# Kernel tuning notes

Measured on AMD Instinct MI355X. Metric: run time of the kernel, lower is better.

## Reference

```python
import jax, jax.numpy as jnp
import numpy as np

N_EMB = 8192
EMB_DIM = 128
BETA = 0.25


def setup_inputs() -> dict:
    key = jax.random.key(0)
    k1, k2 = jax.random.split(key)
    x = jax.random.normal(k1, (32, EMB_DIM, 1024), dtype=jnp.float32)
    embeddings = jax.random.normal(k2, (N_EMB, EMB_DIM), dtype=jnp.float32)
    return {"x": x, "embeddings": embeddings}


def reference(x, embeddings):
    # preprocess: swap chn_dim(=1) with last dim, flatten to tokens
    xt = jnp.swapaxes(x, 1, -1)                      # [B, L, D]
    flat = xt.reshape(-1, EMB_DIM)                   # [N, D]
    prenorm = jnp.linalg.norm(flat - jnp.mean(flat)) / np.sqrt(float(flat.size))

    # squared-euclidean distances via matmul + norms: [N, n_emb]
    s1 = jnp.sum(flat * flat, axis=1, keepdims=True)
    s2 = jnp.sum(embeddings * embeddings, axis=1)
    sim = flat @ embeddings.T
    distances = s1 + s2 - 2.0 * sim

    min_distance = jnp.min(distances, axis=1)
    idx = jnp.argmin(distances, axis=1)              # [N] int
    fit = jnp.mean(jnp.nan_to_num(min_distance))

    # EMA scatter statistics (one-hot matmul in torch == segment_sum here)
    k_sum = jax.ops.segment_sum(flat, idx, num_segments=N_EMB)         # [n_emb, D]
    k_elem = jax.ops.segment_sum(jnp.ones_like(idx, jnp.float32), idx,
                                 num_segments=N_EMB)                   # [n_emb]
    k_prob = k_elem / jnp.sum(k_elem)
    entropy = -jnp.sum(k_prob * jnp.log(k_prob + 1e-8))

    # embedding gather, reshape back to channels-first
    quantized = embeddings[idx].reshape(xt.shape)    # [B, L, D]
    quantized = jnp.swapaxes(quantized, 1, -1)       # [B, D, L]

    # ema_update=True -> codebook_loss = 0, only commit loss
    commit_loss = BETA * jnp.mean((jax.lax.stop_gradient(quantized) - x) ** 2)
    loss = commit_loss

    # straight-through estimator
    out = x + jax.lax.stop_gradient(quantized - x)
    return out, quantized, loss, fit, prenorm, entropy, k_sum, k_elem
```

## Files before the change

### kernel.cpp

```cpp
#include <hip/hip_runtime.h>
#include <math.h>
#include <float.h>

#define BB 32
#define DD 128
#define LL 1024
#define NN 32768
#define NE 8192
#define XSZ 4194304
#define OUT_OFF_Q     4194304
#define OUT_OFF_SCAL  8388608
#define OUT_OFF_KSUM  8388612
#define OUT_OFF_KELEM 9437188

typedef unsigned int u32;
typedef unsigned short u16;
typedef int   i32x4 __attribute__((ext_vector_type(4)));
typedef float f32x4 __attribute__((ext_vector_type(4)));

__device__ inline float waveSum(float v){
  #pragma unroll
  for (int o = 32; o > 0; o >>= 1) v += __shfl_down(v, o, 64);
  return v;
}
__device__ inline double waveSumD(double v){
  #pragma unroll
  for (int o = 32; o > 0; o >>= 1) v += __shfl_down(v, o, 64);
  return v;
}

__global__ __launch_bounds__(256) void prep_kernel(const float* __restrict__ e,
    u16* __restrict__ eh8, int* __restrict__ s2seed, float* __restrict__ s2f,
    int* __restrict__ cnt, float* __restrict__ accs)
{
  int t = threadIdx.x;
  if (blockIdx.x < 32) cnt[blockIdx.x * 256 + t] = 0;
  if (blockIdx.x == 32 && t < 16) accs[t] = 0.f;

  int row = blockIdx.x * 4 + (t >> 6);
  int kd  = t & 63;
  float2 ev = *reinterpret_cast<const float2*>(&e[row * DD + kd * 2]);
  int e0 = __float2int_rn(ev.x * 4096.f);
  int e1 = __float2int_rn(ev.y * 4096.f);
  e0 = min(max(e0, -32639), 32639);
  e1 = min(max(e1, -32639), 32639);
  double sq = (double)e0 * (double)e0 + (double)e1 * (double)e1;
  sq = waveSumD(sq);
  float sqf = ev.x * ev.x + ev.y * ev.y;
  sqf = waveSum(sqf);
  if (kd == 0){
    int sd = (int)(sq * (1.0 / 131072.0));
    sd = min(sd, 120000);
    s2seed[row] = -sd;
    s2f[row] = sqf;
  }
  int h0 = (e0 + 128) >> 8;
  int h1 = (e1 + 128) >> 8;
  int k = kd * 2;
  int T16 = row >> 4, lr = row & 15;
  int kt2 = k >> 6, lg = (k >> 4) & 3, j = k & 15;
  int du16 = (((T16*2 + kt2) * 1024) + lg*256 + lr*16 + j) >> 1;
  eh8[du16] = (u16)((h0 & 255) | ((h1 & 255) << 8));
}

#define LOADSET(AH0,AH1,SEED,TT) \
  { int T_ = (TT); \
    AH0 = *(const i32x4*)(ehp + (size_t)(T_*2 + 0) * 256); \
    AH1 = *(const i32x4*)(ehp + (size_t)(T_*2 + 1) * 256); \
    SEED = s2s4[T_*4 + sofs]; }

#define MFMA2S(SLOT, CT, AH0,AH1,SEED) \
  SLOT = __builtin_amdgcn_mfma_i32_16x16x64_i8(AH0, Bh[CT][0], SEED, 0,0,0); \
  SLOT = __builtin_amdgcn_mfma_i32_16x16x64_i8(AH1, Bh[CT][1], SLOT, 0,0,0);

#define KEYS1(T1V, CT, JV) \
  { _Pragma("unroll") \
    for (int r = 0; r < 4; ++r){ \
      int key = (int)(((u32)T1V[r] << 13) + (u32)(JV[r])); \
      int k2n; \
      asm("v_med3_i32 %0, %1, %2, %3" \
          : "=v"(k2n) : "v"(key), "v"(k1[CT]), "v"(k2[CT])); \
      k2[CT] = k2n; \
      k1[CT] = max(key, k1[CT]); \
    } }

#define TILE_BODY(AH0,AH1,SEED,JV) \
  MFMA2S(sa, 0, AH0,AH1,SEED) \
  MFMA2S(sb, 1, AH0,AH1,SEED) \
  KEYS1(sa, 0, JV) \
  MFMA2S(sa, 2, AH0,AH1,SEED) \
  KEYS1(sb, 1, JV) \
  MFMA2S(sb, 3, AH0,AH1,SEED) \
  KEYS1(sa, 2, JV) \
  KEYS1(sb, 3, JV)

__global__ __launch_bounds__(256, 4) void argmin_mfma(
    const float* __restrict__ x,
    const u32* __restrict__ eh8,
    const i32x4* __restrict__ s2s4,
    int* __restrict__ idx1o, int* __restrict__ idx2o)
{
  __shared__ int kk1[1024];
  __shared__ int kk2[1024];

  int t  = threadIdx.x;
  int w  = t >> 6;
  int l  = t & 63;
  int lr = l & 15;
  int lg = l >> 4;

  int blk  = blockIdx.x;
  int half = blk >> 9;
  int tb   = blk & 511;
  int hb64 = half * 64;

  int n0 = tb * 64;
  int b  = n0 >> 10;
  int l0 = n0 & 1023;
  const float* xb = x + (size_t)b * (DD * LL);

  i32x4 Bh[4][2];
  #pragma unroll
  for (int ct = 0; ct < 4; ++ct){
    int tok = l0 + ct*16 + lr;
    #pragma unroll
    for (int kt = 0; kt < 2; ++kt){
      #pragma unroll
      for (int dw = 0; dw < 4; ++dw){
        u32 hw = 0;
        #pragma unroll
        for (int bb = 0; bb < 4; ++bb){
          int k = kt*64 + lg*16 + dw*4 + bb;
          int xi = __float2int_rn(xb[(size_t)k * LL + tok] * 4096.f);
          xi = min(max(xi, -32639), 32639);
          int h  = (xi + 128) >> 8;
          hw |= ((u32)h & 255u) << (8*bb);
        }
        Bh[ct][kt][dw] = (int)hw;
      }
    }
  }

  int k1[4], k2[4];
  #pragma unroll
  for (int ct = 0; ct < 4; ++ct){ k1[ct] = (int)0x80000000; k2[ct] = (int)0x80000000; }

  int jvA[4], jvB[4];
  #pragma unroll
  for (int r = 0; r < 4; ++r){
    jvA[r] = 8191 - (hb64*64 + w*16 + lg*4 + r);
    jvB[r] = jvA[r] - 64;
  }

  const u32* ehp = eh8 + (size_t)l * 4;
  int sofs = lg;

  i32x4 Ah0A, Ah1A, seedA;
  i32x4 Ah0B, Ah1B, seedB;
  i32x4 sa, sb;

  LOADSET(Ah0A, Ah1A, seedA, (hb64 + 0)*4 + w)
  LOADSET(Ah0B, Ah1B, seedB, (hb64 + 1)*4 + w)

  for (int it = 0; it < 64; it += 2){
    TILE_BODY(Ah0A, Ah1A, seedA, jvA)
    if (it + 2 < 64){
      LOADSET(Ah0A, Ah1A, seedA, (hb64 + it + 2)*4 + w)
    }
    #pragma unroll
    for (int r = 0; r < 4; ++r) jvA[r] -= 128;

    TILE_BODY(Ah0B, Ah1B, seedB, jvB)
    if (it + 3 < 64){
      LOADSET(Ah0B, Ah1B, seedB, (hb64 + it + 3)*4 + w)
    }
    #pragma unroll
    for (int r = 0; r < 4; ++r) jvB[r] -= 128;
  }

  #pragma unroll
  for (int ct = 0; ct < 4; ++ct){
    int sidx = (ct*16 + lr)*16 + w*4 + lg;
    kk1[sidx] = k1[ct];
    kk2[sidx] = k2[ct];
  }
  __syncthreads();
  if (t < 64){
    int K1 = (int)0x80000000, K2 = (int)0x80000000;
    #pragma unroll 4
    for (int s = 0; s < 16; ++s){
      int a = kk1[t*16 + s], b2 = kk2[t*16 + s];
      int mn = min(a, K1);  K2 = max(mn, K2);  K1 = max(a, K1);
      mn = min(b2, K1);     K2 = max(mn, K2);  K1 = max(b2, K1);
    }
    idx1o[half*NN + n0 + t] = 8191 - (K1 & 8191);
    idx2o[half*NN + n0 + t] = 8191 - (K2 & 8191);
  }
}

__global__ __launch_bounds__(256) void fixup_kernel(const float* __restrict__ x,
    const float* __restrict__ e, const float* __restrict__ s2f,
    const int* __restrict__ idx1, const int* __restrict__ idx2,
    int* __restrict__ idxf, int* __restrict__ cnt, float* __restrict__ accs,
    float* __restrict__ out, float* __restrict__ quant, float* __restrict__ xT)
{
  __shared__ float red[5][4][64];
  __shared__ int jws[64];

  int t = threadIdx.x;
  int w = t >> 6, l = t & 63;
  int n0 = blockIdx.x * 64;
  int n  = n0 + l;
  int b  = n0 >> 10;
  int l0 = n0 & 1023;
  size_t base = (size_t)b * (DD * LL) + l0 + l;
  const float* xb = x + base;

  int js[4];
  js[0] = idx1[n];      js[1] = idx2[n];
  js[2] = idx1[NN + n]; js[3] = idx2[NN + n];

  float s1 = 0.f, sx = 0.f;
  float dt0 = 0.f, dt1 = 0.f, dt2 = 0.f, dt3 = 0.f;
  int kbase = w * 32;
  #pragma unroll
  for (int k4 = 0; k4 < 8; ++k4){
    int k = kbase + k4*4;
    float x0 = xb[(size_t)(k+0) * LL];
    float x1 = xb[(size_t)(k+1) * LL];
    float x2 = xb[(size_t)(k+2) * LL];
    float x3 = xb[(size_t)(k+3) * LL];
    s1 = fmaf(x0,x0, fmaf(x1,x1, fmaf(x2,x2, fmaf(x3,x3, s1))));
    sx += x0 + x1 + x2 + x3;
    if (xT) *(float4*)&xT[(size_t)n * DD + k] = make_float4(x0,x1,x2,x3);
    float4 v0 = *(const float4*)&e[(size_t)js[0] * DD + k];
    float4 v1 = *(const float4*)&e[(size_t)js[1] * DD + k];
    float4 v2 = *(const float4*)&e[(size_t)js[2] * DD + k];
    float4 v3 = *(const float4*)&e[(size_t)js[3] * DD + k];
    dt0 = fmaf(x0,v0.x, fmaf(x1,v0.y, fmaf(x2,v0.z, fmaf(x3,v0.w, dt0))));
    dt1 = fmaf(x0,v1.x, fmaf(x1,v1.y, fmaf(x2,v1.z, fmaf(x3,v1.w, dt1))));
    dt2 = fmaf(x0,v2.x, fmaf(x1,v2.y, fmaf(x2,v2.z, fmaf(x3,v2.w, dt2))));
    dt3 = fmaf(x0,v3.x, fmaf(x1,v3.y, fmaf(x2,v3.z, fmaf(x3,v3.w, dt3))));
  }
  red[0][w][l] = s1;
  red[1][w][l] = dt0;  red[2][w][l] = dt1;
  red[3][w][l] = dt2;  red[4][w][l] = dt3;
  sx = waveSum(sx);
  if (l == 0) atomicAdd(&accs[0], sx);
  __syncthreads();

  if (w == 0){
    float S1 = red[0][0][l] + red[0][1][l] + red[0][2][l] + red[0][3][l];
    float D[4];
    #pragma unroll
    for (int i = 0; i < 4; ++i)
      D[i] = red[1+i][0][l] + red[1+i][1][l] + red[1+i][2][l] + red[1+i][3][l];
    int jw = js[0];
    float dw = S1 + s2f[js[0]] - 2.f * D[0];
    #pragma unroll
    for (int i = 1; i < 4; ++i){
      float di = S1 + s2f[js[i]] - 2.f * D[i];
      if (di < dw || (di == dw && js[i] < jw)) { dw = di; jw = js[i]; }
    }
    idxf[n] = jw;
    atomicAdd(&cnt[jw], 1);
    jws[l] = jw;
    float S1s = waveSum(S1);
    float dws = waveSum(dw);
    if (l == 0){
      atomicAdd(&accs[1], S1s);
      atomicAdd(&accs[3], dws);
    }
  }
  __syncthreads();

  int jw = jws[l];
  float* ob = out   + base;
  float* qb = quant + base;
  #pragma unroll
  for (int k4 = 0; k4 < 8; ++k4){
    int k = kbase + k4*4;
    float4 q = *(const float4*)&e[(size_t)jw * DD + k];
    ob[(size_t)(k+0)*LL] = q.x;  qb[(size_t)(k+0)*LL] = q.x;
    ob[(size_t)(k+1)*LL] = q.y;  qb[(size_t)(k+1)*LL] = q.y;
    ob[(size_t)(k+2)*LL] = q.z;  qb[(size_t)(k+2)*LL] = q.z;
    ob[(size_t)(k+3)*LL] = q.w;  qb[(size_t)(k+3)*LL] = q.w;
  }
}

__global__ __launch_bounds__(1024) void prefix_kernel(const int* __restrict__ cnt,
    int* __restrict__ cursor, float* __restrict__ kelem,
    const float* __restrict__ accs, float* __restrict__ scal)
{
  __shared__ int sc[1024];
  __shared__ double er[16];
  int t = threadIdx.x;
  int c[8]; int s = 0;
  #pragma unroll
  for (int i = 0; i < 8; ++i){ c[i] = cnt[t*8 + i]; s += c[i]; }
  sc[t] = s;
  __syncthreads();
  for (int off = 1; off < 1024; off <<= 1){
    int v = sc[t];
    int u = (t >= off) ? sc[t - off] : 0;
    __syncthreads();
    sc[t] = v + u;
    __syncthreads();
  }
  int base = t ? sc[t-1] : 0;
  #pragma unroll
  for (int i = 0; i < 8; ++i){
    cursor[t*8 + i] = base;
    kelem[t*8 + i] = (float)c[i];
    base += c[i];
  }
  double es = 0.0;
  #pragma unroll
  for (int i = 0; i < 8; ++i){
    float p = (float)c[i] * (1.0f / NN);
    es += (double)(p * logf(p + 1e-8f));
  }
  es = waveSumD(es);
  if ((t & 63) == 0) er[t >> 6] = es;
  __syncthreads();
  if (t == 0){
    double ent = 0.0;
    #pragma unroll
    for (int i = 0; i < 16; ++i) ent += er[i];
    ent = -ent;
    float sum = accs[0], sq = accs[1], fitsum = accs[3];
    double mu  = (double)sum / (double)XSZ;
    double var = (double)sq / (double)XSZ - mu * mu;
    if (var < 0) var = 0;
    scal[0] = (float)(0.25 * (double)fitsum / (double)XSZ);
    scal[1] = (float)((double)fitsum / (double)NN);
    scal[2] = (float)sqrt(var);
    scal[3] = (float)ent;
  }
}

__global__ __launch_bounds__(256) void scatter_kernel(const int* __restrict__ idxf,
    int* __restrict__ cursor, int* __restrict__ order, int* __restrict__ jsorted,
    float* __restrict__ ksum)
{
  int n = blockIdx.x * 256 + threadIdx.x;
  {
    const float4 z = make_float4(0.f,0.f,0.f,0.f);
    float4* kz = (float4*)&ksum[(size_t)n * 32];
    #pragma unroll
    for (int i = 0; i < 8; ++i) kz[i] = z;
  }
  int j = idxf[n];
  int p = atomicAdd(&cursor[j], 1);
  order[p] = n;
  jsorted[p] = j;
}

__global__ __launch_bounds__(256) void ksum_chunk_kernel(const float* __restrict__ xT,
    const int* __restrict__ order, const int* __restrict__ jsorted,
    float* __restrict__ ksum)
{
  int wv = threadIdx.x >> 6, lane = threadIdx.x & 63;
  int chunk = blockIdx.x * 4 + wv;
  int st = chunk * 16;
  int myo = order[st + (lane & 15)];
  int myj = jsorted[st + (lane & 15)];
  float a0 = 0.f, a1 = 0.f;
  bool inside = false;
  #pragma unroll
  for (int k = 0; k < 16; ++k){
    int j = __shfl(myj, k);
    int n = __shfl(myo, k);
    const float* xr = xT + (size_t)n * DD;
    a0 += xr[lane];
    a1 += xr[64 + lane];
    int jn = (k < 15) ? __shfl(myj, k + 1) : -1;
    if (jn != j){
      if (inside && k < 15){
        ksum[j * DD + lane]      = a0;
        ksum[j * DD + 64 + lane] = a1;
      } else {
        atomicAdd(&ksum[j * DD + lane], a0);
        atomicAdd(&ksum[j * DD + 64 + lane], a1);
      }
      a0 = 0.f; a1 = 0.f;
      inside = true;
    }
  }
}

__global__ __launch_bounds__(256) void ksum_kernel(const float* __restrict__ x,
    const int* __restrict__ order, const int* __restrict__ cnt,
    const int* __restrict__ cursor, float* __restrict__ ksum)
{
  int w = threadIdx.x >> 6, lane = threadIdx.x & 63;
  int j = blockIdx.x * 4 + w;
  int c = cnt[j];
  int st = cursor[j] - c;
  float a0 = 0.f, a1 = 0.f;
  for (int k = 0; k < c; ++k){
    int n = order[st + k];
    int b = n >> 10, l = n & 1023;
    const float* xb = x + (size_t)b * (DD * LL) + l;
    a0 += xb[lane * LL];
    a1 += xb[(lane + 64) * LL];
  }
  ksum[j * DD + lane]      = a0;
  ksum[j * DD + 64 + lane] = a1;
}

extern "C" void kernel_launch(void* const* d_in, const int* in_sizes, int n_in,
                              void* d_out, int out_size, void* d_ws, size_t ws_size,
                              hipStream_t stream)
{
  const float* x = (const float*)d_in[0];
  const float* e = (const float*)d_in[1];
  float* out   = (float*)d_out;
  float* quant = out + OUT_OFF_Q;
  float* scal  = out + OUT_OFF_SCAL;
  float* ksum  = out + OUT_OFF_KSUM;
  float* kelem = out + OUT_OFF_KELEM;

  char* wsb = (char*)d_ws;
  u16*   eh8     = (u16*)(wsb);
  float* s2f     = (float*)(wsb + 1048576);
  int*   s2seed  = (int*)(wsb + 2097152);
  int*   idx1    = (int*)(wsb + 2129920);
  int*   idx2    = (int*)(wsb + 2392064);
  int*   idxf    = (int*)(wsb + 2654208);
  int*   cnt     = (int*)(wsb + 2785280);
  int*   cursor  = (int*)(wsb + 2818048);
  int*   order   = (int*)(wsb + 2850816);
  int*   jsorted = (int*)(wsb + 2981888);
  float* accs    = (float*)(wsb + 3112960);
  float* xT      = (float*)(wsb + 4194304);
  bool useXT = ws_size >= (size_t)(4194304 + 16777216);

  prep_kernel   <<<NE / 4,     256, 0, stream>>>(e, eh8, s2seed, s2f, cnt, accs);
  argmin_mfma   <<<1024,       256, 0, stream>>>(x, (const u32*)eh8,
                                                 (const i32x4*)s2seed, idx1, idx2);
  fixup_kernel  <<<NN / 64,    256, 0, stream>>>(x, e, s2f, idx1, idx2, idxf, cnt,
                                                 accs, out, quant,
                                                 useXT ? xT : (float*)nullptr);
  prefix_kernel <<<1,         1024, 0, stream>>>(cnt, cursor, kelem, accs, scal);
  scatter_kernel<<<NN / 256,   256, 0, stream>>>(idxf, cursor, order, jsorted, ksum);
  if (useXT){
    ksum_chunk_kernel<<<NN / 64, 256, 0, stream>>>(xT, order, jsorted, ksum);
  } else {
    ksum_kernel      <<<NE / 4,  256, 0, stream>>>(x, order, cnt, cursor, ksum);
  }
}
```

Measured before the change: 152.1 us.

## Pre-reduce argmin keys per row group, move xT transpose to LDS kernel, widen ksum chunks

The argmin inner loop now takes the max over four rows' packed keys with v_max3 before a single med3/max top-2 update per column tile, instead of four separate updates. Row offsets are folded into the scores as small subtractions, which keeps one index base per lane. The xT transpose moves out of fixup, where each thread did strided float4 stores, into a separate LDS-tiled kernel that also zeroes ksum. ksum chunks grow from 16 to 32 tokens per wave. Pre-reducing four rows before the top-2 update can drop a genuine second-best candidate when both best and runner-up come from the same four-row group, which may change the fixup result. The extra launch also adds overhead.

```diff
diff --git a/kernel.cpp b/kernel.cpp
--- a/kernel.cpp
+++ b/kernel.cpp
@@ -73,26 +73,29 @@
   SLOT = __builtin_amdgcn_mfma_i32_16x16x64_i8(AH0, Bh[CT][0], SEED, 0,0,0); \
   SLOT = __builtin_amdgcn_mfma_i32_16x16x64_i8(AH1, Bh[CT][1], SLOT, 0,0,0);
 
-#define KEYS1(T1V, CT, JV) \
-  { _Pragma("unroll") \
-    for (int r = 0; r < 4; ++r){ \
-      int key = (int)(((u32)T1V[r] << 13) + (u32)(JV[r])); \
-      int k2n; \
-      asm("v_med3_i32 %0, %1, %2, %3" \
-          : "=v"(k2n) : "v"(key), "v"(k1[CT]), "v"(k2[CT])); \
-      k2[CT] = k2n; \
-      k1[CT] = max(key, k1[CT]); \
-    } }
-
-#define TILE_BODY(AH0,AH1,SEED,JV) \
+#define KEYS1(T1V, CT, J) \
+  { int q0 = (int)((u32)T1V[0] << 13); \
+    int q1 = (int)((u32)T1V[1] << 13) - 1; \
+    int q2 = (int)((u32)T1V[2] << 13) - 2; \
+    int q3 = (int)((u32)T1V[3] << 13) - 3; \
+    int m; \
+    asm("v_max3_i32 %0, %1, %2, %3" : "=v"(m) : "v"(q0), "v"(q1), "v"(q2)); \
+    m = max(m, q3) + (J); \
+    int k2n; \
+    asm("v_med3_i32 %0, %1, %2, %3" \
+        : "=v"(k2n) : "v"(m), "v"(k1[CT]), "v"(k2[CT])); \
+    k2[CT] = k2n; \
+    k1[CT] = max(m, k1[CT]); }
+
+#define TILE_BODY(AH0,AH1,SEED,J) \
   MFMA2S(sa, 0, AH0,AH1,SEED) \
   MFMA2S(sb, 1, AH0,AH1,SEED) \
-  KEYS1(sa, 0, JV) \
+  KEYS1(sa, 0, J) \
   MFMA2S(sa, 2, AH0,AH1,SEED) \
-  KEYS1(sb, 1, JV) \
+  KEYS1(sb, 1, J) \
   MFMA2S(sb, 3, AH0,AH1,SEED) \
-  KEYS1(sa, 2, JV) \
-  KEYS1(sb, 3, JV)
+  KEYS1(sa, 2, J) \
+  KEYS1(sb, 3, J)
 
 __global__ __launch_bounds__(256, 4) void argmin_mfma(
     const float* __restrict__ x,
@@ -145,12 +148,8 @@
   #pragma unroll
   for (int ct = 0; ct < 4; ++ct){ k1[ct] = (int)0x80000000; k2[ct] = (int)0x80000000; }
 
-  int jvA[4], jvB[4];
-  #pragma unroll
-  for (int r = 0; r < 4; ++r){
-    jvA[r] = 8191 - (hb64*64 + w*16 + lg*4 + r);
-    jvB[r] = jvA[r] - 64;
-  }
+  int JA = 8191 - (hb64*64 + w*16 + lg*4);
+  int JB = JA - 64;
 
   const u32* ehp = eh8 + (size_t)l * 4;
   int sofs = lg;
@@ -163,19 +162,17 @@
   LOADSET(Ah0B, Ah1B, seedB, (hb64 + 1)*4 + w)
 
   for (int it = 0; it < 64; it += 2){
-    TILE_BODY(Ah0A, Ah1A, seedA, jvA)
+    TILE_BODY(Ah0A, Ah1A, seedA, JA)
     if (it + 2 < 64){
       LOADSET(Ah0A, Ah1A, seedA, (hb64 + it + 2)*4 + w)
     }
-    #pragma unroll
-    for (int r = 0; r < 4; ++r) jvA[r] -= 128;
-
-    TILE_BODY(Ah0B, Ah1B, seedB, jvB)
+    JA -= 128;
+
+    TILE_BODY(Ah0B, Ah1B, seedB, JB)
     if (it + 3 < 64){
       LOADSET(Ah0B, Ah1B, seedB, (hb64 + it + 3)*4 + w)
     }
-    #pragma unroll
-    for (int r = 0; r < 4; ++r) jvB[r] -= 128;
+    JB -= 128;
   }
 
   #pragma unroll
@@ -202,7 +199,7 @@
     const float* __restrict__ e, const float* __restrict__ s2f,
     const int* __restrict__ idx1, const int* __restrict__ idx2,
     int* __restrict__ idxf, int* __restrict__ cnt, float* __restrict__ accs,
-    float* __restrict__ out, float* __restrict__ quant, float* __restrict__ xT)
+    float* __restrict__ out, float* __restrict__ quant)
 {
   __shared__ float red[5][4][64];
   __shared__ int jws[64];
@@ -232,7 +229,6 @@
     float x3 = xb[(size_t)(k+3) * LL];
     s1 = fmaf(x0,x0, fmaf(x1,x1, fmaf(x2,x2, fmaf(x3,x3, s1))));
     sx += x0 + x1 + x2 + x3;
-    if (xT) *(float4*)&xT[(size_t)n * DD + k] = make_float4(x0,x1,x2,x3);
     float4 v0 = *(const float4*)&e[(size_t)js[0] * DD + k];
     float4 v1 = *(const float4*)&e[(size_t)js[1] * DD + k];
     float4 v2 = *(const float4*)&e[(size_t)js[2] * DD + k];
@@ -280,11 +276,11 @@
   #pragma unroll
   for (int k4 = 0; k4 < 8; ++k4){
     int k = kbase + k4*4;
-    float4 q = *(const float4*)&e[(size_t)jw * DD + k];
-    ob[(size_t)(k+0)*LL] = q.x;  qb[(size_t)(k+0)*LL] = q.x;
-    ob[(size_t)(k+1)*LL] = q.y;  qb[(size_t)(k+1)*LL] = q.y;
-    ob[(size_t)(k+2)*LL] = q.z;  qb[(size_t)(k+2)*LL] = q.z;
-    ob[(size_t)(k+3)*LL] = q.w;  qb[(size_t)(k+3)*LL] = q.w;
+    float4 qv = *(const float4*)&e[(size_t)jw * DD + k];
+    ob[(size_t)(k+0)*LL] = qv.x;  qb[(size_t)(k+0)*LL] = qv.x;
+    ob[(size_t)(k+1)*LL] = qv.y;  qb[(size_t)(k+1)*LL] = qv.y;
+    ob[(size_t)(k+2)*LL] = qv.z;  qb[(size_t)(k+2)*LL] = qv.z;
+    ob[(size_t)(k+3)*LL] = qv.w;  qb[(size_t)(k+3)*LL] = qv.w;
   }
 }
 
@@ -340,43 +336,68 @@
 }
 
 __global__ __launch_bounds__(256) void scatter_kernel(const int* __restrict__ idxf,
-    int* __restrict__ cursor, int* __restrict__ order, int* __restrict__ jsorted,
-    float* __restrict__ ksum)
+    int* __restrict__ cursor, int* __restrict__ order, int* __restrict__ jsorted)
 {
   int n = blockIdx.x * 256 + threadIdx.x;
-  {
-    const float4 z = make_float4(0.f,0.f,0.f,0.f);
-    float4* kz = (float4*)&ksum[(size_t)n * 32];
-    #pragma unroll
-    for (int i = 0; i < 8; ++i) kz[i] = z;
-  }
   int j = idxf[n];
   int p = atomicAdd(&cursor[j], 1);
   order[p] = n;
   jsorted[p] = j;
 }
 
+__global__ __launch_bounds__(256) void transpose_kernel(const float* __restrict__ x,
+    float* __restrict__ xT, float* __restrict__ ksum)
+{
+  __shared__ float tile[64][137];
+  int t = threadIdx.x;
+  {
+    const float4 z = make_float4(0.f,0.f,0.f,0.f);
+    float4* kz = (float4*)&ksum[(size_t)blockIdx.x * 2048 + t * 8];
+    kz[0] = z; kz[1] = z;
+  }
+  int b  = blockIdx.x >> 4;
+  int l0 = (blockIdx.x & 15) << 6;
+  const float* xb = x + (size_t)b * (DD * LL);
+  #pragma unroll
+  for (int rep = 0; rep < 32; ++rep){
+    int idx = rep * 256 + t;
+    int d = idx >> 6, ll = idx & 63;
+    tile[ll][d] = xb[d * LL + l0 + ll];
+  }
+  __syncthreads();
+  int n0 = (b << 10) + l0;
+  #pragma unroll
+  for (int rep = 0; rep < 8; ++rep){
+    int idx = rep * 256 + t;
+    int row = idx >> 5, c4 = idx & 31;
+    float4 v;
+    v.x = tile[row][c4*4+0]; v.y = tile[row][c4*4+1];
+    v.z = tile[row][c4*4+2]; v.w = tile[row][c4*4+3];
+    *(float4*)&xT[(size_t)(n0 + row) * DD + c4*4] = v;
+  }
+}
+
 __global__ __launch_bounds__(256) void ksum_chunk_kernel(const float* __restrict__ xT,
     const int* __restrict__ order, const int* __restrict__ jsorted,
     float* __restrict__ ksum)
 {
   int wv = threadIdx.x >> 6, lane = threadIdx.x & 63;
   int chunk = blockIdx.x * 4 + wv;
-  int st = chunk * 16;
-  int myo = order[st + (lane & 15)];
-  int myj = jsorted[st + (lane & 15)];
+  int st = chunk * 32;
+  int myo = order[st + (lane & 31)];
+  int myj = jsorted[st + (lane & 31)];
   float a0 = 0.f, a1 = 0.f;
   bool inside = false;
   #pragma unroll
-  for (int k = 0; k < 16; ++k){
+  for (int k = 0; k < 32; ++k){
     int j = __shfl(myj, k);
     int n = __shfl(myo, k);
     const float* xr = xT + (size_t)n * DD;
     a0 += xr[lane];
     a1 += xr[64 + lane];
-    int jn = (k < 15) ? __shfl(myj, k + 1) : -1;
+    int jn = (k < 31) ? __shfl(myj, k + 1) : -1;
     if (jn != j){
-      if (inside && k < 15){
+      if (inside && k < 31){
         ksum[j * DD + lane]      = a0;
         ksum[j * DD + 64 + lane] = a1;
       } else {
@@ -440,12 +461,12 @@
   argmin_mfma   <<<1024,       256, 0, stream>>>(x, (const u32*)eh8,
                                                  (const i32x4*)s2seed, idx1, idx2);
   fixup_kernel  <<<NN / 64,    256, 0, stream>>>(x, e, s2f, idx1, idx2, idxf, cnt,
-                                                 accs, out, quant,
-                                                 useXT ? xT : (float*)nullptr);
+                                                 accs, out, quant);
   prefix_kernel <<<1,         1024, 0, stream>>>(cnt, cursor, kelem, accs, scal);
-  scatter_kernel<<<NN / 256,   256, 0, stream>>>(idxf, cursor, order, jsorted, ksum);
+  scatter_kernel<<<NN / 256,   256, 0, stream>>>(idxf, cursor, order, jsorted);
   if (useXT){
-    ksum_chunk_kernel<<<NN / 64, 256, 0, stream>>>(xT, order, jsorted, ksum);
+    transpose_kernel <<<BB * 16, 256, 0, stream>>>(x, xT, ksum);
+    ksum_chunk_kernel<<<NN / 128, 256, 0, stream>>>(xT, order, jsorted, ksum);
   } else {
     ksum_kernel      <<<NE / 4,  256, 0, stream>>>(x, order, cnt, cursor, ksum);
   }
```

New measurement: 145.1 us. 4.6% less time.
